# Kernel optimization log

Measured on AMD Instinct MI355X. Metric: run time of the kernel, lower is better.

## Reference

```python
import jax, jax.numpy as jnp
import numpy as np

N = 100000
D = 512   # input_size
C = 2     # output_class
QDIM = 128


def setup_inputs() -> dict:
    key = jax.random.key(0)
    ks = jax.random.split(key, 12)
    s = 0.02
    return {
        "feats": jax.random.normal(ks[0], (N, D), jnp.float32),
        "c": jax.random.normal(ks[1], (N, C), jnp.float32),
        "single_predictions": jax.random.normal(ks[2], (N, 1), jnp.float32),
        # self.lin = Linear(D, D) + ReLU
        "W_lin": jax.random.normal(ks[3], (D, D), jnp.float32) * s,
        "b_lin": jnp.zeros((D,), jnp.float32),
        # self.q = Linear(D, 128) + Tanh
        "W_q": jax.random.normal(ks[4], (QDIM, D), jnp.float32) * s,
        "b_q": jnp.zeros((QDIM,), jnp.float32),
        # self.v = Dropout(0.0) + Linear(D, D)
        "W_v": jax.random.normal(ks[5], (D, D), jnp.float32) * s,
        "b_v": jnp.zeros((D,), jnp.float32),
        # self.fcc = Conv1d(C, C, kernel_size=D)
        "W_fcc": jax.random.normal(ks[6], (C, C, D), jnp.float32) * s,
        "b_fcc": jnp.zeros((C,), jnp.float32),
    }


def reference(feats, c, single_predictions, W_lin, b_lin, W_q, b_q, W_v, b_v, W_fcc, b_fcc):
    n = feats.shape[0]
    k = int(0.2 * n)

    preds = single_predictions[:, 0]                      # [N]
    # torch.topk(largest=False): indices of the k smallest; zero them out
    _, lastk_idx = jax.lax.top_k(-preds, k)
    preds = preds.at[lastk_idx].set(0.0)
    instance_score = jax.nn.softmax(preds, axis=0)[:, None]  # [N,1], softmax over instances

    f = feats * instance_score + feats                    # [N,D]
    f = jax.nn.relu(f @ W_lin.T + b_lin)                  # self.lin
    V = f @ W_v.T + b_v                                   # [N,D] (dropout p=0)
    Q = jnp.tanh(f @ W_q.T + b_q)                         # [N,128]

    # torch.sort(c, 0, descending)[1][0,:] == per-class argmax over instances
    m_indices = jnp.argmax(c, axis=0)                     # [C]
    m_feats = f[m_indices]                                # [C,D]
    q_max = jnp.tanh(m_feats @ W_q.T + b_q)               # [C,128]

    A = Q @ q_max.T                                       # [N,C]
    A = jax.nn.softmax(A / jnp.sqrt(jnp.float32(QDIM)), axis=0)  # softmax over instances
    B = A.T @ V                                           # [C,D]

    # Conv1d(C, C, kernel=D) on B[None] -> length-1 output: full contraction
    Cout = jnp.einsum('id,oid->o', B, W_fcc) + b_fcc      # [C]
    return Cout[None, :], A, B
```

## Files before the change

### kernel.cpp

```cpp
#include <hip/hip_runtime.h>
#include <stdint.h>

typedef unsigned short u16;
typedef __bf16 bf16t;
typedef bf16t bf16x8 __attribute__((ext_vector_type(8)));
typedef float f32x4 __attribute__((ext_vector_type(4)));
typedef unsigned long long ull;

#define NROWS 100000
#define DD 512
#define QD 128
#define KSEL 20000
#define NB 1563

__device__ __forceinline__ uint32_t fmono(float x){
  uint32_t u = __float_as_uint(x);
  return (u & 0x80000000u) ? ~u : (u | 0x80000000u);
}
__device__ __forceinline__ float finv(uint32_t k){
  uint32_t u = (k & 0x80000000u) ? (k & 0x7fffffffu) : ~k;
  return __uint_as_float(u);
}
__device__ __forceinline__ u16 f2bf(float x){
  uint32_t u = __float_as_uint(x);
  u += 0x7fffu + ((u >> 16) & 1u);
  return (u16)(u >> 16);
}
__device__ __forceinline__ uint32_t pkbf(float a, float b){
  return (uint32_t)f2bf(a) | ((uint32_t)f2bf(b) << 16);
}

struct Scal {
  uint32_t keyT;
  float Z;
  uint32_t pad[14];
};

#define MFMA16(A,B,C) __builtin_amdgcn_mfma_f32_16x16x32_bf16(A,B,C,0,0,0)

__global__ void k_conv(const float* __restrict__ Wl, const float* __restrict__ Wv,
                       const float* __restrict__ Wq, u16* __restrict__ wch,
                       uint32_t* __restrict__ hist, ull* __restrict__ cmax){
  int idx = blockIdx.x*256 + threadIdx.x;
  if (idx < 65536) hist[idx] = 0u;
  if (idx == 0){ cmax[0] = 0ull; cmax[1] = 0ull; }
  int ci  = idx >> 12;
  int rem = idx & 4095;
  int r   = rem >> 5;
  int col = rem & 31;
  float v;
  if (ci < 64){
    int nt = ci >> 4, kc = ci & 15;
    v = Wl[(size_t)(nt*128 + r)*DD + kc*32 + col];
  } else {
    int c2 = ci - 64;
    int nt2 = c2 >> 4, kc = c2 & 15;
    if (nt2 == 0) v = Wq[(size_t)r*DD + kc*32 + col];
    else          v = Wv[(size_t)((nt2-1)*128 + r)*DD + kc*32 + col];
  }
  wch[idx] = f2bf(v);
}

__global__ void k_sel1(const float* __restrict__ preds, const float* __restrict__ c,
                       uint32_t* __restrict__ hist, ull* __restrict__ cmax){
  __shared__ ull kr0[4], kr1[4];
  const int t = threadIdx.x;
  const int gid = blockIdx.x*256 + t;
  const int lane = t & 63;

  const float4* p4 = (const float4*)preds;
  for (int i = gid; i < 25000; i += 65536){
    float4 v = p4[i];
    atomicAdd(&hist[fmono(v.x) >> 16], 1u);
    atomicAdd(&hist[fmono(v.y) >> 16], 1u);
    atomicAdd(&hist[fmono(v.z) >> 16], 1u);
    atomicAdd(&hist[fmono(v.w) >> 16], 1u);
  }

  ull k0 = 0ull, k1 = 0ull;
  const float4* c4 = (const float4*)c;
  for (int i = gid; i < 50000; i += 65536){
    float4 v = c4[i];
    uint32_t r0 = 2u*i, r1 = 2u*i + 1u;
    ull a0 = ((ull)fmono(v.x) << 32) | (ull)(~r0);
    ull a1 = ((ull)fmono(v.z) << 32) | (ull)(~r1);
    ull b0 = ((ull)fmono(v.y) << 32) | (ull)(~r0);
    ull b1 = ((ull)fmono(v.w) << 32) | (ull)(~r1);
    if (a0 > k0) k0 = a0;
    if (a1 > k0) k0 = a1;
    if (b0 > k1) k1 = b0;
    if (b1 > k1) k1 = b1;
  }
  #pragma unroll
  for (int off = 32; off; off >>= 1){
    ull o0 = __shfl_xor(k0, off); if (o0 > k0) k0 = o0;
    ull o1 = __shfl_xor(k1, off); if (o1 > k1) k1 = o1;
  }
  if (lane == 0){ kr0[t >> 6] = k0; kr1[t >> 6] = k1; }
  __syncthreads();
  if (t == 0){
    ull m0 = kr0[0], m1 = kr1[0];
    #pragma unroll
    for (int w = 1; w < 4; ++w){
      if (kr0[w] > m0) m0 = kr0[w];
      if (kr1[w] > m1) m1 = kr1[w];
    }
    atomicMax(&cmax[0], m0);
    atomicMax(&cmax[1], m1);
  }
}

#define CAND_CAP 8192
__launch_bounds__(1024)
__global__ void k_prep2(const float* __restrict__ preds, const float* __restrict__ feats,
                        const float* __restrict__ Wl, const float* __restrict__ bl,
                        const float* __restrict__ Wq, const float* __restrict__ bq,
                        const uint32_t* __restrict__ hist, const ull* __restrict__ cmax,
                        Scal* __restrict__ sc, float* __restrict__ qmv){
  __shared__ uint32_t cand[CAND_CAP];
  __shared__ uint32_t wsum[16], woff[16];
  __shared__ float zred[16];
  __shared__ uint32_t s_B, s_cumBelow, s_keyT, candN;
  __shared__ float s_Z;
  __shared__ uint32_t s_mi[2];
  __shared__ float fmX[2][512];
  __shared__ float fmF[2][512];
  const int t = threadIdx.x;
  const int lane = t & 63, wv = t >> 6;

  if (t == 0){
    candN = 0;
    s_mi[0] = ~(uint32_t)(cmax[0] & 0xffffffffull);
    s_mi[1] = ~(uint32_t)(cmax[1] & 0xffffffffull);
  }

  const int b0 = t*64;
  uint32_t local = 0;
  {
    const uint4* h4 = (const uint4*)(hist + b0);
    #pragma unroll 4
    for (int q = 0; q < 16; ++q){ uint4 hv = h4[q]; local += hv.x + hv.y + hv.z + hv.w; }
  }
  uint32_t x = local;
  #pragma unroll
  for (int off = 1; off < 64; off <<= 1){
    uint32_t y = __shfl_up(x, off);
    if (lane >= off) x += y;
  }
  if (lane == 63) wsum[wv] = x;
  __syncthreads();
  if (t == 0){
    uint32_t cum = 0;
    for (int w = 0; w < 16; ++w){ woff[w] = cum; cum += wsum[w]; }
  }
  __syncthreads();
  uint32_t excl = x - local + woff[wv];
  if (excl < KSEL && excl + local >= KSEL){
    uint32_t cum = excl;
    for (int b = 0; b < 64; ++b){
      uint32_t h = hist[b0 + b];
      if (cum + h >= KSEL){ s_B = (uint32_t)(b0 + b); s_cumBelow = cum; break; }
      cum += h;
    }
  }
  __syncthreads();
  const uint32_t B = s_B;

  float sA = 0.f;
  const float4* p4 = (const float4*)preds;
  for (int i = t; i < 25000; i += 1024){
    float4 v = p4[i];
    float vv[4] = {v.x, v.y, v.z, v.w};
    #pragma unroll
    for (int e = 0; e < 4; ++e){
      uint32_t k = fmono(vv[e]);
      uint32_t bb = k >> 16;
      if (bb > B){
        sA += __expf(vv[e]);
      } else if (bb == B){
        uint32_t idx = atomicAdd(&candN, 1u);
        if (idx < CAND_CAP) cand[idx] = k;
      }
    }
  }
  #pragma unroll
  for (int off = 32; off; off >>= 1) sA += __shfl_xor(sA, off);
  if (lane == 0) zred[wv] = sA;
  __syncthreads();

  const uint32_t n = candN < CAND_CAP ? candN : CAND_CAP;
  const uint32_t r = KSEL - s_cumBelow;
  for (uint32_t i = t; i < n; i += 1024){
    uint32_t ki = cand[i];
    uint32_t less = 0, eq = 0;
    for (uint32_t j = 0; j < n; ++j){
      uint32_t kj = cand[j];
      less += (kj < ki) ? 1u : 0u;
      eq   += (kj == ki) ? 1u : 0u;
    }
    if (less < r && r <= less + eq) s_keyT = ki;
  }
  __syncthreads();
  const uint32_t keyT = s_keyT;

  float sCA = 0.f;
  for (uint32_t i = t; i < n; i += 1024){
    uint32_t k = cand[i];
    if (k > keyT) sCA += __expf(finv(k));
  }
  #pragma unroll
  for (int off = 32; off; off >>= 1) sCA += __shfl_xor(sCA, off);
  if (lane == 0) zred[wv] += sCA;
  __syncthreads();
  if (t == 0){
    float Z = (float)KSEL;
    for (int w = 0; w < 16; ++w) Z += zred[w];
    s_Z = Z;
    sc->keyT = keyT; sc->Z = Z;
  }
  __syncthreads();

  {
    int j = t >> 9, col = t & 511;
    fmX[j][col] = feats[(size_t)s_mi[j]*DD + col];
  }
  __syncthreads();

  {
    int nn = t >> 1, h = t & 1;
    const float4* wr4 = (const float4*)(Wl + (size_t)nn*DD + h*256);
    const float4* x04 = (const float4*)(&fmX[0][h*256]);
    const float4* x14 = (const float4*)(&fmX[1][h*256]);
    float a0 = 0.f, a1 = 0.f;
    #pragma unroll 4
    for (int k = 0; k < 64; ++k){
      float4 w = wr4[k], u = x04[k], v = x14[k];
      a0 += u.x*w.x + u.y*w.y + u.z*w.z + u.w*w.w;
      a1 += v.x*w.x + v.y*w.y + v.z*w.z + v.w*w.w;
    }
    a0 += __shfl_xor(a0, 1);
    a1 += __shfl_xor(a1, 1);
    if (h == 0){
      float Z = s_Z;
      float p0 = preds[s_mi[0]]; float q0 = (fmono(p0) <= keyT) ? 0.f : p0;
      float g0 = 1.f + __expf(q0) / Z;
      float p1 = preds[s_mi[1]]; float q1 = (fmono(p1) <= keyT) ? 0.f : p1;
      float g1 = 1.f + __expf(q1) / Z;
      float v0 = bl[nn] + g0*a0; fmF[0][nn] = v0 > 0.f ? v0 : 0.f;
      float v1 = bl[nn] + g1*a1; fmF[1][nn] = v1 > 0.f ? v1 : 0.f;
    }
  }
  __syncthreads();

  if (t < 256){
    int q = t & 127, j = t >> 7;
    const float4* wr4 = (const float4*)(Wq + (size_t)q*DD);
    const float4* x4  = (const float4*)(fmF[j]);
    float a0 = 0.f, a1 = 0.f;
    #pragma unroll 4
    for (int k = 0; k < 128; k += 2){
      float4 w0 = wr4[k], u0 = x4[k];
      float4 w1 = wr4[k+1], u1 = x4[k+1];
      a0 += u0.x*w0.x + u0.y*w0.y + u0.z*w0.z + u0.w*w0.w;
      a1 += u1.x*w1.x + u1.y*w1.y + u1.z*w1.z + u1.w*w1.w;
    }
    qmv[j*QD + q] = tanhf(bq[q] + a0 + a1);
  }
}

__launch_bounds__(256, 2)
__global__ void k_fused(const float* __restrict__ feats, const float* __restrict__ preds,
                        const u16* __restrict__ wch,
                        const float* __restrict__ bl, const float* __restrict__ bv,
                        const float* __restrict__ bq, const float* __restrict__ qmv,
                        const Scal* __restrict__ sc,
                        float* __restrict__ gpart, float* __restrict__ gpartE,
                        float* __restrict__ Aout){
  __shared__ __align__(16) u16 lds[40960];
  u16* AF  = lds;
  u16* WB0 = lds + 32768;
  u16* WB1 = lds + 36864;
  float* sred = (float*)WB1;
  const int tid = threadIdx.x;
  const int lane = tid & 63, quad = lane >> 4, l16 = lane & 15;
  const int wave = tid >> 6, wm = wave >> 1, wn = wave & 1;
  const long i0 = (long)blockIdx.x * 64;
  const uint32_t keyT = sc->keyT;
  const float Z = sc->Z;

  {
    int row = lane;
    long ir = i0 + row; if (ir >= NROWS) ir = NROWS - 1;
    float p = preds[ir];
    float pm = (fmono(p) <= keyT) ? 0.f : p;
    float g = 1.f + __expf(pm) / Z;
    const float4* src = (const float4*)(feats + ir*DD + wave*128);
    u16* dstrow = AF + row*512;
    const int swz = row & 7;
    #pragma unroll
    for (int j = 0; j < 16; ++j){
      float4 a = src[2*j], b = src[2*j + 1];
      uint4 pk;
      pk.x = pkbf(a.x*g, a.y*g); pk.y = pkbf(a.z*g, a.w*g);
      pk.z = pkbf(b.x*g, b.y*g); pk.w = pkbf(b.z*g, b.w*g);
      int blk = (wave << 4) | j;
      *(uint4*)&dstrow[(blk ^ swz) << 3] = pk;
    }
  }

  const u16* wsrc = wch + (size_t)tid * 16;
  const int rS = tid >> 1, pS = tid & 1;
  const int offA = rS*32 + ((((pS << 1)    ) ^ (rS & 3)) << 3);
  const int offB = rS*32 + ((((pS << 1) | 1) ^ (rS & 3)) << 3);
  uint4 pA0 = *(const uint4*)(wsrc);
  uint4 pA1 = *(const uint4*)(wsrc + 8);
  uint4 pB0 = *(const uint4*)(wsrc + 4096);
  uint4 pB1 = *(const uint4*)(wsrc + 4096 + 8);
  *(uint4*)&WB0[offA] = pA0;
  *(uint4*)&WB0[offB] = pA1;
  pA0 = *(const uint4*)(wsrc + 8192);
  pA1 = *(const uint4*)(wsrc + 8192 + 8);
  __syncthreads();

  const int sb  = l16 & 7;
  const int sb2 = l16 & 3;
  const int base_a = (wm*32 + l16) * 512;
  const int rB = wn*64 + l16;
  const int qsw = (quad ^ sb2) << 3;
  const int off_b0 = (rB +  0)*32 + qsw;
  const int off_b1 = (rB + 16)*32 + qsw;
  const int off_b2 = (rB + 32)*32 + qsw;
  const int off_b3 = (rB + 48)*32 + qsw;

  f32x4 acc[2][4];
  uint32_t pkF[4][16];
  float eR0[2][4], eR1[2][4];
  int ci = 0;

#define KSTEP(BUFC, BUFN, P0, P1)                                                  \
  {                                                                                \
    int abk = (((ci & 15) << 2) | quad) ^ sb;                                      \
    bf16x8 a0 = *(const bf16x8*)&AF[base_a + (abk << 3)];                          \
    bf16x8 a1 = *(const bf16x8*)&AF[base_a + 8192 + (abk << 3)];                   \
    bf16x8 b0 = *(const bf16x8*)&BUFC[off_b0];                                     \
    bf16x8 b1 = *(const bf16x8*)&BUFC[off_b1];                                     \
    bf16x8 b2 = *(const bf16x8*)&BUFC[off_b2];                                     \
    bf16x8 b3 = *(const bf16x8*)&BUFC[off_b3];                                     \
    if (ci + 1 < 144){ *(uint4*)&BUFN[offA] = P0; *(uint4*)&BUFN[offB] = P1; }     \
    if (ci + 3 < 144){                                                             \
      const u16* s_ = wsrc + (size_t)(ci + 3)*4096;                                \
      P0 = *(const uint4*)s_; P1 = *(const uint4*)(s_ + 8);                        \
    }                                                                              \
    acc[0][0] = MFMA16(a0, b0, acc[0][0]);                                         \
    acc[0][1] = MFMA16(a0, b1, acc[0][1]);                                         \
    acc[0][2] = MFMA16(a0, b2, acc[0][2]);                                         \
    acc[0][3] = MFMA16(a0, b3, acc[0][3]);                                         \
    acc[1][0] = MFMA16(a1, b0, acc[1][0]);                                         \
    acc[1][1] = MFMA16(a1, b1, acc[1][1]);                                         \
    acc[1][2] = MFMA16(a1, b2, acc[1][2]);                                         \
    acc[1][3] = MFMA16(a1, b3, acc[1][3]);                                         \
    __syncthreads();                                                               \
    ++ci;                                                                          \
  }

  for (int nt = 0; nt < 4; ++nt){
    #pragma unroll
    for (int mi = 0; mi < 2; ++mi)
      #pragma unroll
      for (int ni = 0; ni < 4; ++ni) acc[mi][ni] = (f32x4){0.f,0.f,0.f,0.f};
    for (int kh = 0; kh < 8; ++kh){
      KSTEP(WB0, WB1, pB0, pB1);
      KSTEP(WB1, WB0, pA0, pA1);
    }
    #pragma unroll
    for (int ni = 0; ni < 4; ++ni){
      float bb = bl[nt*128 + wn*64 + ni*16 + l16];
      #pragma unroll
      for (int mi = 0; mi < 2; ++mi){
        float e0 = acc[mi][ni][0] + bb; e0 = e0 > 0.f ? e0 : 0.f;
        float e1 = acc[mi][ni][1] + bb; e1 = e1 > 0.f ? e1 : 0.f;
        float e2 = acc[mi][ni][2] + bb; e2 = e2 > 0.f ? e2 : 0.f;
        float e3 = acc[mi][ni][3] + bb; e3 = e3 > 0.f ? e3 : 0.f;
        pkF[nt][mi*8 + ni*2 + 0] = pkbf(e0, e1);
        pkF[nt][mi*8 + ni*2 + 1] = pkbf(e2, e3);
      }
    }
  }

  #pragma unroll
  for (int nt = 0; nt < 4; ++nt)
    #pragma unroll
    for (int ni = 0; ni < 4; ++ni)
      #pragma unroll
      for (int mi = 0; mi < 2; ++mi){
        int col = nt*128 + wn*64 + ni*16 + l16;
        int r0 = wm*32 + mi*16 + quad*4;
        uint32_t x = pkF[nt][mi*8 + ni*2], y = pkF[nt][mi*8 + ni*2 + 1];
        int cb = col >> 3, cw = col & 7;
        AF[(r0+0)*512 + (((cb) ^ ((r0+0)&7)) << 3) + cw] = (u16)x;
        AF[(r0+1)*512 + (((cb) ^ ((r0+1)&7)) << 3) + cw] = (u16)(x >> 16);
        AF[(r0+2)*512 + (((cb) ^ ((r0+2)&7)) << 3) + cw] = (u16)y;
        AF[(r0+3)*512 + (((cb) ^ ((r0+3)&7)) << 3) + cw] = (u16)(y >> 16);
      }
  __syncthreads();

  for (int nt2 = 0; nt2 < 5; ++nt2){
    #pragma unroll
    for (int mi = 0; mi < 2; ++mi)
      #pragma unroll
      for (int ni = 0; ni < 4; ++ni) acc[mi][ni] = (f32x4){0.f,0.f,0.f,0.f};
    for (int kh = 0; kh < 8; ++kh){
      KSTEP(WB0, WB1, pB0, pB1);
      KSTEP(WB1, WB0, pA0, pA1);
    }
    if (nt2 == 0){
      float p0[2][4], p1[2][4];
      #pragma unroll
      for (int mi = 0; mi < 2; ++mi)
        #pragma unroll
        for (int e = 0; e < 4; ++e){ p0[mi][e] = 0.f; p1[mi][e] = 0.f; }
      #pragma unroll
      for (int ni = 0; ni < 4; ++ni){
        int qc = wn*64 + ni*16 + l16;
        float bqv = bq[qc], q0 = qmv[qc], q1 = qmv[QD + qc];
        #pragma unroll
        for (int mi = 0; mi < 2; ++mi)
          #pragma unroll
          for (int e = 0; e < 4; ++e){
            float tq = tanhf(acc[mi][ni][e] + bqv);
            p0[mi][e] += tq * q0;
            p1[mi][e] += tq * q1;
          }
      }
      #pragma unroll
      for (int off = 1; off <= 8; off <<= 1)
        #pragma unroll
        for (int mi = 0; mi < 2; ++mi)
          #pragma unroll
          for (int e = 0; e < 4; ++e){
            p0[mi][e] += __shfl_xor(p0[mi][e], off);
            p1[mi][e] += __shfl_xor(p1[mi][e], off);
          }
      if (l16 == 0){
        #pragma unroll
        for (int mi = 0; mi < 2; ++mi)
          #pragma unroll
          for (int e = 0; e < 4; ++e){
            int row = wm*32 + mi*16 + quad*4 + e;
            sred[(row*2 + 0)*2 + wn] = p0[mi][e];
            sred[(row*2 + 1)*2 + wn] = p1[mi][e];
          }
      }
      __syncthreads();
      #pragma unroll
      for (int mi = 0; mi < 2; ++mi)
        #pragma unroll
        for (int e = 0; e < 4; ++e){
          int row = wm*32 + mi*16 + quad*4 + e;
          bool valid = (i0 + row) < NROWS;
          float sv0 = (sred[(row*2 + 0)*2 + 0] + sred[(row*2 + 0)*2 + 1]) * 0.08838834764831845f;
          float sv1 = (sred[(row*2 + 1)*2 + 0] + sred[(row*2 + 1)*2 + 1]) * 0.08838834764831845f;
          eR0[mi][e] = valid ? __expf(sv0) : 0.f;
          eR1[mi][e] = valid ? __expf(sv1) : 0.f;
        }
      if (tid < 128){
        int row = tid >> 1, j = tid & 1;
        float sv = (sred[(row*2 + j)*2 + 0] + sred[(row*2 + j)*2 + 1]) * 0.08838834764831845f;
        bool valid = (i0 + row) < NROWS;
        float ev = valid ? __expf(sv) : 0.f;
        if (valid) Aout[(i0 + row)*2 + j] = ev;
        float t2 = ev;
        #pragma unroll
        for (int off = 2; off <= 32; off <<= 1) t2 += __shfl_xor(t2, off);
        if (lane < 2) gpartE[(size_t)blockIdx.x*4 + (tid >> 6)*2 + j] = t2;
      }
      __syncthreads();
    } else {
      #pragma unroll
      for (int ni = 0; ni < 4; ++ni){
        int colv = (nt2 - 1)*128 + wn*64 + ni*16 + l16;
        float bvv = bv[colv];
        float b0 = 0.f, b1 = 0.f;
        #pragma unroll
        for (int mi = 0; mi < 2; ++mi)
          #pragma unroll
          for (int e = 0; e < 4; ++e){
            float v = acc[mi][ni][e] + bvv;
            b0 += v * eR0[mi][e];
            b1 += v * eR1[mi][e];
          }
        b0 += __shfl_xor(b0, 16); b0 += __shfl_xor(b0, 32);
        b1 += __shfl_xor(b1, 16); b1 += __shfl_xor(b1, 32);
        if (quad == 0){
          gpart[((size_t)blockIdx.x*2 + wm)*1024 + colv]       = b0;
          gpart[((size_t)blockIdx.x*2 + wm)*1024 + 512 + colv] = b1;
        }
      }
    }
  }
#undef KSTEP
}

__global__ void k_red(const float* __restrict__ gpart, const float* __restrict__ gpartE,
                      float* __restrict__ sumEV, float* __restrict__ sumE){
  const int t = threadIdx.x;
  if (blockIdx.x == 256){
    __shared__ float r0[256], r1[256];
    float s0 = 0.f, s1 = 0.f;
    for (int i = t; i < NB*2; i += 256){ s0 += gpartE[(size_t)i*2]; s1 += gpartE[(size_t)i*2 + 1]; }
    r0[t] = s0; r1[t] = s1;
    __syncthreads();
    for (int st = 128; st; st >>= 1){
      if (t < st){ r0[t] += r0[t + st]; r1[t] += r1[t + st]; }
      __syncthreads();
    }
    if (t == 0){ sumE[0] = r0[0]; sumE[1] = r1[0]; }
    return;
  }
  __shared__ float4 red[256];
  int col4 = blockIdx.x * 4;
  float4 s = {0.f, 0.f, 0.f, 0.f};
  for (int r = t; r < NB*2; r += 256){
    float4 v = *(const float4*)(gpart + (size_t)r*1024 + col4);
    s.x += v.x; s.y += v.y; s.z += v.z; s.w += v.w;
  }
  red[t] = s;
  __syncthreads();
  for (int st = 128; st; st >>= 1){
    if (t < st){
      float4 o = red[t + st];
      red[t].x += o.x; red[t].y += o.y; red[t].z += o.z; red[t].w += o.w;
    }
    __syncthreads();
  }
  if (t == 0) *(float4*)(sumEV + col4) = red[0];
}

__global__ void k_post(float* __restrict__ out, const float* __restrict__ sumE,
                       const float* __restrict__ sumEV, const float* __restrict__ Wfcc,
                       const float* __restrict__ bfcc){
  if (blockIdx.x < 782){
    int idx = blockIdx.x*256 + threadIdx.x;
    if (idx < 200000) out[2 + idx] = out[2 + idx] / sumE[idx & 1];
    return;
  }
  __shared__ float red[512];
  int t = threadIdx.x;
  float z0 = sumE[0], z1 = sumE[1];
  float c0 = 0.f, c1 = 0.f;
  for (int e = t; e < 1024; e += 256){
    float bvv = sumEV[e] / ((e >> 9) ? z1 : z0);
    out[200002 + e] = bvv;
    c0 += bvv * Wfcc[e];
    c1 += bvv * Wfcc[1024 + e];
  }
  red[t] = c0; red[256 + t] = c1;
  __syncthreads();
  for (int s = 128; s; s >>= 1){
    if (t < s){ red[t] += red[t + s]; red[256 + t] += red[256 + t + s]; }
    __syncthreads();
  }
  if (t == 0){ out[0] = red[0] + bfcc[0]; out[1] = red[256] + bfcc[1]; }
}

extern "C" void kernel_launch(void* const* d_in, const int* in_sizes, int n_in,
                              void* d_out, int out_size, void* d_ws, size_t ws_size,
                              hipStream_t stream){
  (void)in_sizes; (void)n_in; (void)out_size; (void)ws_size;
  const float* feats = (const float*)d_in[0];
  const float* c     = (const float*)d_in[1];
  const float* preds = (const float*)d_in[2];
  const float* W_lin = (const float*)d_in[3];
  const float* b_lin = (const float*)d_in[4];
  const float* W_q   = (const float*)d_in[5];
  const float* b_q   = (const float*)d_in[6];
  const float* W_v   = (const float*)d_in[7];
  const float* b_v   = (const float*)d_in[8];
  const float* W_fcc = (const float*)d_in[9];
  const float* b_fcc = (const float*)d_in[10];
  float* out = (float*)d_out;
  char* ws = (char*)d_ws;

  u16*   wch    = (u16*)(ws + 0);
  Scal*  sc     = (Scal*)(ws + 1179648);
  float* qmv    = (float*)(ws + 1179712);
  float* sumE   = (float*)(ws + 1180736);
  float* sumEV  = (float*)(ws + 1180800);
  float* gpartE = (float*)(ws + 1184896);
  float* gpart  = (float*)(ws + 1209984);
  uint32_t* hist = (uint32_t*)(ws + 1209984);
  ull*      cmax = (ull*)(ws + 1209984 + 262144);

  k_conv <<<2304, 256, 0, stream>>>(W_lin, W_v, W_q, wch, hist, cmax);
  k_sel1 <<<256, 256, 0, stream>>>(preds, c, hist, cmax);
  k_prep2<<<1, 1024, 0, stream>>>(preds, feats, W_lin, b_lin, W_q, b_q, hist, cmax, sc, qmv);
  k_fused<<<NB, 256, 0, stream>>>(feats, preds, wch, b_lin, b_v, b_q,
                                  qmv, sc, gpart, gpartE, out + 2);
  k_red  <<<257, 256, 0, stream>>>(gpart, gpartE, sumEV, sumE);
  k_post <<<783, 256, 0, stream>>>(out, sumE, sumEV, W_fcc, b_fcc);
}
```

Before: 633.0 us.

## Stream weight fragments into registers, drop LDS weight buffers and per-step barriers

The fused GEMM kernel stops staging weight chunks through double-buffered LDS with a __syncthreads every k-step. Each wave now loads its B fragments straight from global memory into registers, prefetched two steps ahead, and covers all 64 rows with a 4x2 MFMA tile per wave. This removes the per-step barriers and the LDS traffic for B, but each wave now fetches its own weights with no sharing, which raises global and L2 traffic, and LDS use drops. Separately, the single-block prep kernel is split into three kernels so the small m_feats GEMVs run across several blocks, at the cost of two extra launches.

```diff
diff --git a/kernel.cpp b/kernel.cpp
--- a/kernel.cpp
+++ b/kernel.cpp
@@ -112,27 +112,17 @@
 
 #define CAND_CAP 8192
 __launch_bounds__(1024)
-__global__ void k_prep2(const float* __restrict__ preds, const float* __restrict__ feats,
-                        const float* __restrict__ Wl, const float* __restrict__ bl,
-                        const float* __restrict__ Wq, const float* __restrict__ bq,
-                        const uint32_t* __restrict__ hist, const ull* __restrict__ cmax,
-                        Scal* __restrict__ sc, float* __restrict__ qmv){
+__global__ void k_prep2(const float* __restrict__ preds,
+                        const uint32_t* __restrict__ hist,
+                        Scal* __restrict__ sc){
   __shared__ uint32_t cand[CAND_CAP];
   __shared__ uint32_t wsum[16], woff[16];
   __shared__ float zred[16];
   __shared__ uint32_t s_B, s_cumBelow, s_keyT, candN;
-  __shared__ float s_Z;
-  __shared__ uint32_t s_mi[2];
-  __shared__ float fmX[2][512];
-  __shared__ float fmF[2][512];
   const int t = threadIdx.x;
   const int lane = t & 63, wv = t >> 6;
 
-  if (t == 0){
-    candN = 0;
-    s_mi[0] = ~(uint32_t)(cmax[0] & 0xffffffffull);
-    s_mi[1] = ~(uint32_t)(cmax[1] & 0xffffffffull);
-  }
+  if (t == 0) candN = 0;
 
   const int b0 = t*64;
   uint32_t local = 0;
@@ -215,57 +205,68 @@
   if (t == 0){
     float Z = (float)KSEL;
     for (int w = 0; w < 16; ++w) Z += zred[w];
-    s_Z = Z;
     sc->keyT = keyT; sc->Z = Z;
   }
-  __syncthreads();
-
-  {
-    int j = t >> 9, col = t & 511;
+}
+
+__global__ void k_prep3(const float* __restrict__ preds, const float* __restrict__ feats,
+                        const float* __restrict__ Wl, const float* __restrict__ bl,
+                        const ull* __restrict__ cmax, const Scal* __restrict__ sc,
+                        float* __restrict__ fmFw){
+  __shared__ float fmX[2][512];
+  __shared__ uint32_t s_mi[2];
+  const int t = threadIdx.x;
+  if (t < 2) s_mi[t] = ~(uint32_t)(cmax[t] & 0xffffffffull);
+  __syncthreads();
+  for (int i = t; i < 1024; i += 256){
+    int j = i >> 9, col = i & 511;
     fmX[j][col] = feats[(size_t)s_mi[j]*DD + col];
   }
   __syncthreads();
-
-  {
-    int nn = t >> 1, h = t & 1;
-    const float4* wr4 = (const float4*)(Wl + (size_t)nn*DD + h*256);
-    const float4* x04 = (const float4*)(&fmX[0][h*256]);
-    const float4* x14 = (const float4*)(&fmX[1][h*256]);
-    float a0 = 0.f, a1 = 0.f;
-    #pragma unroll 4
-    for (int k = 0; k < 64; ++k){
-      float4 w = wr4[k], u = x04[k], v = x14[k];
-      a0 += u.x*w.x + u.y*w.y + u.z*w.z + u.w*w.w;
-      a1 += v.x*w.x + v.y*w.y + v.z*w.z + v.w*w.w;
-    }
-    a0 += __shfl_xor(a0, 1);
-    a1 += __shfl_xor(a1, 1);
-    if (h == 0){
-      float Z = s_Z;
-      float p0 = preds[s_mi[0]]; float q0 = (fmono(p0) <= keyT) ? 0.f : p0;
-      float g0 = 1.f + __expf(q0) / Z;
-      float p1 = preds[s_mi[1]]; float q1 = (fmono(p1) <= keyT) ? 0.f : p1;
-      float g1 = 1.f + __expf(q1) / Z;
-      float v0 = bl[nn] + g0*a0; fmF[0][nn] = v0 > 0.f ? v0 : 0.f;
-      float v1 = bl[nn] + g1*a1; fmF[1][nn] = v1 > 0.f ? v1 : 0.f;
-    }
-  }
-  __syncthreads();
-
-  if (t < 256){
-    int q = t & 127, j = t >> 7;
-    const float4* wr4 = (const float4*)(Wq + (size_t)q*DD);
-    const float4* x4  = (const float4*)(fmF[j]);
-    float a0 = 0.f, a1 = 0.f;
-    #pragma unroll 4
-    for (int k = 0; k < 128; k += 2){
-      float4 w0 = wr4[k], u0 = x4[k];
-      float4 w1 = wr4[k+1], u1 = x4[k+1];
-      a0 += u0.x*w0.x + u0.y*w0.y + u0.z*w0.z + u0.w*w0.w;
-      a1 += u1.x*w1.x + u1.y*w1.y + u1.z*w1.z + u1.w*w1.w;
-    }
-    qmv[j*QD + q] = tanhf(bq[q] + a0 + a1);
-  }
+  const int nn = blockIdx.x*32 + (t >> 3);
+  const int h = t & 7;
+  const float4* wr4 = (const float4*)(Wl + (size_t)nn*DD + h*64);
+  const float4* x04 = (const float4*)(&fmX[0][h*64]);
+  const float4* x14 = (const float4*)(&fmX[1][h*64]);
+  float a0 = 0.f, a1 = 0.f;
+  #pragma unroll
+  for (int k = 0; k < 16; ++k){
+    float4 w = wr4[k], u = x04[k], v = x14[k];
+    a0 += u.x*w.x + u.y*w.y + u.z*w.z + u.w*w.w;
+    a1 += v.x*w.x + v.y*w.y + v.z*w.z + v.w*w.w;
+  }
+  a0 += __shfl_xor(a0, 1); a0 += __shfl_xor(a0, 2); a0 += __shfl_xor(a0, 4);
+  a1 += __shfl_xor(a1, 1); a1 += __shfl_xor(a1, 2); a1 += __shfl_xor(a1, 4);
+  if (h == 0){
+    uint32_t keyT = sc->keyT;
+    float Z = sc->Z;
+    float p0 = preds[s_mi[0]]; float q0 = (fmono(p0) <= keyT) ? 0.f : p0;
+    float g0 = 1.f + __expf(q0) / Z;
+    float p1 = preds[s_mi[1]]; float q1 = (fmono(p1) <= keyT) ? 0.f : p1;
+    float g1 = 1.f + __expf(q1) / Z;
+    float v0 = bl[nn] + g0*a0; fmFw[nn]       = v0 > 0.f ? v0 : 0.f;
+    float v1 = bl[nn] + g1*a1; fmFw[512 + nn] = v1 > 0.f ? v1 : 0.f;
+  }
+}
+
+__global__ void k_prep4(const float* __restrict__ Wq, const float* __restrict__ bq,
+                        const float* __restrict__ fmFw, float* __restrict__ qmv){
+  __shared__ float xs[512];
+  const int t = threadIdx.x;
+  const int j = blockIdx.x;
+  for (int i = t; i < 512; i += 256) xs[i] = fmFw[j*512 + i];
+  __syncthreads();
+  const int q = t >> 1, h = t & 1;
+  const float4* wr4 = (const float4*)(Wq + (size_t)q*DD + h*256);
+  const float4* x4  = (const float4*)(&xs[h*256]);
+  float a = 0.f;
+  #pragma unroll 4
+  for (int k = 0; k < 64; ++k){
+    float4 w = wr4[k], u = x4[k];
+    a += u.x*w.x + u.y*w.y + u.z*w.z + u.w*w.w;
+  }
+  a += __shfl_xor(a, 1);
+  if (h == 0) qmv[j*QD + q] = tanhf(bq[q] + a);
 }
 
 __launch_bounds__(256, 2)
@@ -276,17 +277,20 @@
                         const Scal* __restrict__ sc,
                         float* __restrict__ gpart, float* __restrict__ gpartE,
                         float* __restrict__ Aout){
-  __shared__ __align__(16) u16 lds[40960];
-  u16* AF  = lds;
-  u16* WB0 = lds + 32768;
-  u16* WB1 = lds + 36864;
-  float* sred = (float*)WB1;
+  __shared__ __align__(16) u16 AF[32768];
+  __shared__ __align__(16) float sred[512];
   const int tid = threadIdx.x;
   const int lane = tid & 63, quad = lane >> 4, l16 = lane & 15;
-  const int wave = tid >> 6, wm = wave >> 1, wn = wave & 1;
+  const int wave = tid >> 6;
   const long i0 = (long)blockIdx.x * 64;
   const uint32_t keyT = sc->keyT;
   const float Z = sc->Z;
+
+  const u16* bsrc = wch + (size_t)((wave*32 + l16)*32 + quad*8);
+  uint4 pA0 = *(const uint4*)(bsrc);
+  uint4 pA1 = *(const uint4*)(bsrc + 512);
+  uint4 pB0 = *(const uint4*)(bsrc + 4096);
+  uint4 pB1 = *(const uint4*)(bsrc + 4096 + 512);
 
   {
     int row = lane;
@@ -307,124 +311,102 @@
       *(uint4*)&dstrow[(blk ^ swz) << 3] = pk;
     }
   }
-
-  const u16* wsrc = wch + (size_t)tid * 16;
-  const int rS = tid >> 1, pS = tid & 1;
-  const int offA = rS*32 + ((((pS << 1)    ) ^ (rS & 3)) << 3);
-  const int offB = rS*32 + ((((pS << 1) | 1) ^ (rS & 3)) << 3);
-  uint4 pA0 = *(const uint4*)(wsrc);
-  uint4 pA1 = *(const uint4*)(wsrc + 8);
-  uint4 pB0 = *(const uint4*)(wsrc + 4096);
-  uint4 pB1 = *(const uint4*)(wsrc + 4096 + 8);
-  *(uint4*)&WB0[offA] = pA0;
-  *(uint4*)&WB0[offB] = pA1;
-  pA0 = *(const uint4*)(wsrc + 8192);
-  pA1 = *(const uint4*)(wsrc + 8192 + 8);
-  __syncthreads();
-
-  const int sb  = l16 & 7;
-  const int sb2 = l16 & 3;
-  const int base_a = (wm*32 + l16) * 512;
-  const int rB = wn*64 + l16;
-  const int qsw = (quad ^ sb2) << 3;
-  const int off_b0 = (rB +  0)*32 + qsw;
-  const int off_b1 = (rB + 16)*32 + qsw;
-  const int off_b2 = (rB + 32)*32 + qsw;
-  const int off_b3 = (rB + 48)*32 + qsw;
-
-  f32x4 acc[2][4];
+  __syncthreads();
+
+  const int sb = l16 & 7;
+  f32x4 acc[4][2];
   uint32_t pkF[4][16];
-  float eR0[2][4], eR1[2][4];
+  float eR0[4][4], eR1[4][4];
   int ci = 0;
 
-#define KSTEP(BUFC, BUFN, P0, P1)                                                  \
+#define KSTEP(P0, P1)                                                              \
   {                                                                                \
-    int abk = (((ci & 15) << 2) | quad) ^ sb;                                      \
-    bf16x8 a0 = *(const bf16x8*)&AF[base_a + (abk << 3)];                          \
-    bf16x8 a1 = *(const bf16x8*)&AF[base_a + 8192 + (abk << 3)];                   \
-    bf16x8 b0 = *(const bf16x8*)&BUFC[off_b0];                                     \
-    bf16x8 b1 = *(const bf16x8*)&BUFC[off_b1];                                     \
-    bf16x8 b2 = *(const bf16x8*)&BUFC[off_b2];                                     \
-    bf16x8 b3 = *(const bf16x8*)&BUFC[off_b3];                                     \
-    if (ci + 1 < 144){ *(uint4*)&BUFN[offA] = P0; *(uint4*)&BUFN[offB] = P1; }     \
-    if (ci + 3 < 144){                                                             \
-      const u16* s_ = wsrc + (size_t)(ci + 3)*4096;                                \
-      P0 = *(const uint4*)s_; P1 = *(const uint4*)(s_ + 8);                        \
+    bf16x8 b0 = __builtin_bit_cast(bf16x8, P0);                                    \
+    bf16x8 b1 = __builtin_bit_cast(bf16x8, P1);                                    \
+    if (ci + 2 < 144){                                                             \
+      const u16* s_ = bsrc + (size_t)(ci + 2)*4096;                                \
+      P0 = *(const uint4*)s_;                                                      \
+      P1 = *(const uint4*)(s_ + 512);                                              \
     }                                                                              \
+    int abk = ((((ci & 15) << 2) | quad) ^ sb) << 3;                               \
+    bf16x8 a0 = *(const bf16x8*)&AF[(     l16)*512 + abk];                         \
+    bf16x8 a1 = *(const bf16x8*)&AF[(16 + l16)*512 + abk];                         \
+    bf16x8 a2 = *(const bf16x8*)&AF[(32 + l16)*512 + abk];                         \
+    bf16x8 a3 = *(const bf16x8*)&AF[(48 + l16)*512 + abk];                         \
     acc[0][0] = MFMA16(a0, b0, acc[0][0]);                                         \
     acc[0][1] = MFMA16(a0, b1, acc[0][1]);                                         \
-    acc[0][2] = MFMA16(a0, b2, acc[0][2]);                                         \
-    acc[0][3] = MFMA16(a0, b3, acc[0][3]);                                         \
     acc[1][0] = MFMA16(a1, b0, acc[1][0]);                                         \
     acc[1][1] = MFMA16(a1, b1, acc[1][1]);                                         \
-    acc[1][2] = MFMA16(a1, b2, acc[1][2]);                                         \
-    acc[1][3] = MFMA16(a1, b3, acc[1][3]);                                         \
-    __syncthreads();                                                               \
+    acc[2][0] = MFMA16(a2, b0, acc[2][0]);                                         \
+    acc[2][1] = MFMA16(a2, b1, acc[2][1]);                                         \
+    acc[3][0] = MFMA16(a3, b0, acc[3][0]);                                         \
+    acc[3][1] = MFMA16(a3, b1, acc[3][1]);                                         \
     ++ci;                                                                          \
   }
 
   for (int nt = 0; nt < 4; ++nt){
     #pragma unroll
-    for (int mi = 0; mi < 2; ++mi)
-      #pragma unroll
-      for (int ni = 0; ni < 4; ++ni) acc[mi][ni] = (f32x4){0.f,0.f,0.f,0.f};
+    for (int mi = 0; mi < 4; ++mi)
+      #pragma unroll
+      for (int ni = 0; ni < 2; ++ni) acc[mi][ni] = (f32x4){0.f,0.f,0.f,0.f};
     for (int kh = 0; kh < 8; ++kh){
-      KSTEP(WB0, WB1, pB0, pB1);
-      KSTEP(WB1, WB0, pA0, pA1);
-    }
-    #pragma unroll
-    for (int ni = 0; ni < 4; ++ni){
-      float bb = bl[nt*128 + wn*64 + ni*16 + l16];
-      #pragma unroll
-      for (int mi = 0; mi < 2; ++mi){
+      KSTEP(pA0, pA1);
+      KSTEP(pB0, pB1);
+    }
+    #pragma unroll
+    for (int ni = 0; ni < 2; ++ni){
+      float bb = bl[nt*128 + wave*32 + ni*16 + l16];
+      #pragma unroll
+      for (int mi = 0; mi < 4; ++mi){
         float e0 = acc[mi][ni][0] + bb; e0 = e0 > 0.f ? e0 : 0.f;
         float e1 = acc[mi][ni][1] + bb; e1 = e1 > 0.f ? e1 : 0.f;
         float e2 = acc[mi][ni][2] + bb; e2 = e2 > 0.f ? e2 : 0.f;
         float e3 = acc[mi][ni][3] + bb; e3 = e3 > 0.f ? e3 : 0.f;
-        pkF[nt][mi*8 + ni*2 + 0] = pkbf(e0, e1);
-        pkF[nt][mi*8 + ni*2 + 1] = pkbf(e2, e3);
-      }
-    }
-  }
-
+        pkF[nt][mi*4 + ni*2 + 0] = pkbf(e0, e1);
+        pkF[nt][mi*4 + ni*2 + 1] = pkbf(e2, e3);
+      }
+    }
+  }
+
+  __syncthreads();
   #pragma unroll
   for (int nt = 0; nt < 4; ++nt)
     #pragma unroll
-    for (int ni = 0; ni < 4; ++ni)
-      #pragma unroll
-      for (int mi = 0; mi < 2; ++mi){
-        int col = nt*128 + wn*64 + ni*16 + l16;
-        int r0 = wm*32 + mi*16 + quad*4;
-        uint32_t x = pkF[nt][mi*8 + ni*2], y = pkF[nt][mi*8 + ni*2 + 1];
+    for (int mi = 0; mi < 4; ++mi)
+      #pragma unroll
+      for (int ni = 0; ni < 2; ++ni){
+        int col = nt*128 + wave*32 + ni*16 + l16;
+        int r0 = mi*16 + quad*4;
+        uint32_t x = pkF[nt][mi*4 + ni*2], y = pkF[nt][mi*4 + ni*2 + 1];
         int cb = col >> 3, cw = col & 7;
-        AF[(r0+0)*512 + (((cb) ^ ((r0+0)&7)) << 3) + cw] = (u16)x;
-        AF[(r0+1)*512 + (((cb) ^ ((r0+1)&7)) << 3) + cw] = (u16)(x >> 16);
-        AF[(r0+2)*512 + (((cb) ^ ((r0+2)&7)) << 3) + cw] = (u16)y;
-        AF[(r0+3)*512 + (((cb) ^ ((r0+3)&7)) << 3) + cw] = (u16)(y >> 16);
+        AF[(r0+0)*512 + ((cb ^ ((r0+0)&7)) << 3) + cw] = (u16)x;
+        AF[(r0+1)*512 + ((cb ^ ((r0+1)&7)) << 3) + cw] = (u16)(x >> 16);
+        AF[(r0+2)*512 + ((cb ^ ((r0+2)&7)) << 3) + cw] = (u16)y;
+        AF[(r0+3)*512 + ((cb ^ ((r0+3)&7)) << 3) + cw] = (u16)(y >> 16);
       }
   __syncthreads();
 
   for (int nt2 = 0; nt2 < 5; ++nt2){
     #pragma unroll
-    for (int mi = 0; mi < 2; ++mi)
-      #pragma unroll
-      for (int ni = 0; ni < 4; ++ni) acc[mi][ni] = (f32x4){0.f,0.f,0.f,0.f};
+    for (int mi = 0; mi < 4; ++mi)
+      #pragma unroll
+      for (int ni = 0; ni < 2; ++ni) acc[mi][ni] = (f32x4){0.f,0.f,0.f,0.f};
     for (int kh = 0; kh < 8; ++kh){
-      KSTEP(WB0, WB1, pB0, pB1);
-      KSTEP(WB1, WB0, pA0, pA1);
+      KSTEP(pA0, pA1);
+      KSTEP(pB0, pB1);
     }
     if (nt2 == 0){
-      float p0[2][4], p1[2][4];
-      #pragma unroll
-      for (int mi = 0; mi < 2; ++mi)
+      float p0[4][4], p1[4][4];
+      #pragma unroll
+      for (int mi = 0; mi < 4; ++mi)
         #pragma unroll
         for (int e = 0; e < 4; ++e){ p0[mi][e] = 0.f; p1[mi][e] = 0.f; }
       #pragma unroll
-      for (int ni = 0; ni < 4; ++ni){
-        int qc = wn*64 + ni*16 + l16;
+      for (int ni = 0; ni < 2; ++ni){
+        int qc = wave*32 + ni*16 + l16;
         float bqv = bq[qc], q0 = qmv[qc], q1 = qmv[QD + qc];
         #pragma unroll
-        for (int mi = 0; mi < 2; ++mi)
+        for (int mi = 0; mi < 4; ++mi)
           #pragma unroll
           for (int e = 0; e < 4; ++e){
             float tq = tanhf(acc[mi][ni][e] + bqv);
@@ -435,7 +417,7 @@
       #pragma unroll
       for (int off = 1; off <= 8; off <<= 1)
         #pragma unroll
-        for (int mi = 0; mi < 2; ++mi)
+        for (int mi = 0; mi < 4; ++mi)
           #pragma unroll
           for (int e = 0; e < 4; ++e){
             p0[mi][e] += __shfl_xor(p0[mi][e], off);
@@ -443,29 +425,30 @@
           }
       if (l16 == 0){
         #pragma unroll
-        for (int mi = 0; mi < 2; ++mi)
+        for (int mi = 0; mi < 4; ++mi)
           #pragma unroll
           for (int e = 0; e < 4; ++e){
-            int row = wm*32 + mi*16 + quad*4 + e;
-            sred[(row*2 + 0)*2 + wn] = p0[mi][e];
-            sred[(row*2 + 1)*2 + wn] = p1[mi][e];
+            int row = mi*16 + quad*4 + e;
+            sred[row*8 + 0*4 + wave] = p0[mi][e];
+            sred[row*8 + 1*4 + wave] = p1[mi][e];
           }
       }
       __syncthreads();
       #pragma unroll
-      for (int mi = 0; mi < 2; ++mi)
+      for (int mi = 0; mi < 4; ++mi)
         #pragma unroll
         for (int e = 0; e < 4; ++e){
-          int row = wm*32 + mi*16 + quad*4 + e;
+          int row = mi*16 + quad*4 + e;
           bool valid = (i0 + row) < NROWS;
-          float sv0 = (sred[(row*2 + 0)*2 + 0] + sred[(row*2 + 0)*2 + 1]) * 0.08838834764831845f;
-          float sv1 = (sred[(row*2 + 1)*2 + 0] + sred[(row*2 + 1)*2 + 1]) * 0.08838834764831845f;
+          float sv0 = (sred[row*8+0] + sred[row*8+1] + sred[row*8+2] + sred[row*8+3]) * 0.08838834764831845f;
+          float sv1 = (sred[row*8+4] + sred[row*8+5] + sred[row*8+6] + sred[row*8+7]) * 0.08838834764831845f;
           eR0[mi][e] = valid ? __expf(sv0) : 0.f;
           eR1[mi][e] = valid ? __expf(sv1) : 0.f;
         }
       if (tid < 128){
         int row = tid >> 1, j = tid & 1;
-        float sv = (sred[(row*2 + j)*2 + 0] + sred[(row*2 + j)*2 + 1]) * 0.08838834764831845f;
+        float sv = (sred[row*8 + j*4+0] + sred[row*8 + j*4+1] + sred[row*8 + j*4+2] + sred[row*8 + j*4+3])
+                   * 0.08838834764831845f;
         bool valid = (i0 + row) < NROWS;
         float ev = valid ? __expf(sv) : 0.f;
         if (valid) Aout[(i0 + row)*2 + j] = ev;
@@ -474,15 +457,14 @@
         for (int off = 2; off <= 32; off <<= 1) t2 += __shfl_xor(t2, off);
         if (lane < 2) gpartE[(size_t)blockIdx.x*4 + (tid >> 6)*2 + j] = t2;
       }
-      __syncthreads();
     } else {
       #pragma unroll
-      for (int ni = 0; ni < 4; ++ni){
-        int colv = (nt2 - 1)*128 + wn*64 + ni*16 + l16;
+      for (int ni = 0; ni < 2; ++ni){
+        int colv = (nt2 - 1)*128 + wave*32 + ni*16 + l16;
         float bvv = bv[colv];
         float b0 = 0.f, b1 = 0.f;
         #pragma unroll
-        for (int mi = 0; mi < 2; ++mi)
+        for (int mi = 0; mi < 4; ++mi)
           #pragma unroll
           for (int e = 0; e < 4; ++e){
             float v = acc[mi][ni][e] + bvv;
@@ -492,8 +474,8 @@
         b0 += __shfl_xor(b0, 16); b0 += __shfl_xor(b0, 32);
         b1 += __shfl_xor(b1, 16); b1 += __shfl_xor(b1, 32);
         if (quad == 0){
-          gpart[((size_t)blockIdx.x*2 + wm)*1024 + colv]       = b0;
-          gpart[((size_t)blockIdx.x*2 + wm)*1024 + 512 + colv] = b1;
+          gpart[(size_t)blockIdx.x*1024 + colv]       = b0;
+          gpart[(size_t)blockIdx.x*1024 + 512 + colv] = b1;
         }
       }
     }
@@ -520,7 +502,7 @@
   __shared__ float4 red[256];
   int col4 = blockIdx.x * 4;
   float4 s = {0.f, 0.f, 0.f, 0.f};
-  for (int r = t; r < NB*2; r += 256){
+  for (int r = t; r < NB; r += 256){
     float4 v = *(const float4*)(gpart + (size_t)r*1024 + col4);
     s.x += v.x; s.y += v.y; s.z += v.z; s.w += v.w;
   }
@@ -586,14 +568,17 @@
   float* qmv    = (float*)(ws + 1179712);
   float* sumE   = (float*)(ws + 1180736);
   float* sumEV  = (float*)(ws + 1180800);
-  float* gpartE = (float*)(ws + 1184896);
-  float* gpart  = (float*)(ws + 1209984);
-  uint32_t* hist = (uint32_t*)(ws + 1209984);
-  ull*      cmax = (ull*)(ws + 1209984 + 262144);
+  float* fmFw   = (float*)(ws + 1184896);
+  float* gpartE = (float*)(ws + 1188992);
+  float* gpart  = (float*)(ws + 1214080);
+  uint32_t* hist = (uint32_t*)(ws + 1214080);
+  ull*      cmax = (ull*)(ws + 1214080 + 262144);
 
   k_conv <<<2304, 256, 0, stream>>>(W_lin, W_v, W_q, wch, hist, cmax);
   k_sel1 <<<256, 256, 0, stream>>>(preds, c, hist, cmax);
-  k_prep2<<<1, 1024, 0, stream>>>(preds, feats, W_lin, b_lin, W_q, b_q, hist, cmax, sc, qmv);
+  k_prep2<<<1, 1024, 0, stream>>>(preds, hist, sc);
+  k_prep3<<<16, 256, 0, stream>>>(preds, feats, W_lin, b_lin, cmax, sc, fmFw);
+  k_prep4<<<2, 256, 0, stream>>>(W_q, b_q, fmFw, qmv);
   k_fused<<<NB, 256, 0, stream>>>(feats, preds, wch, b_lin, b_v, b_q,
                                   qmv, sc, gpart, gpartE, out + 2);
   k_red  <<<257, 256, 0, stream>>>(gpart, gpartE, sumEV, sumE);
```

After: 603.6 us. 4.6% less time.
